# Kernel tuning notes

Hardware: AMD Instinct MI355X
Metric: run time of the kernel (lower is better)

The kernel has to match this reference:

```python
import jax, jax.numpy as jnp
import numpy as np

J = 29  # joints per frame (from fc = Linear(29*3, 2))
C = 3   # feature channels (GCNConv(3, 3))


def setup_inputs() -> dict:
    key = jax.random.key(0)
    ks = jax.random.split(key, 6)
    batch_size, num_frames = 256, 1024
    n_total = batch_size * num_frames * J
    x = jax.random.normal(ks[0], (n_total, C), dtype=jnp.float32)
    edge_index = jax.random.randint(ks[1], (2, 56), 0, J, dtype=jnp.int64)
    # GCNConv(3,3) params and fc Linear(87,2) params
    W = jax.random.normal(ks[2], (C, C), dtype=jnp.float32) / np.sqrt(C)
    b = jnp.zeros((C,), dtype=jnp.float32)
    fc_W = jax.random.normal(ks[3], (J * C, 2), dtype=jnp.float32) / np.sqrt(J * C)
    fc_b = jnp.zeros((2,), dtype=jnp.float32)
    return {"x": x, "edge_index": edge_index, "batch_size": batch_size,
            "num_frames": num_frames, "W": W, "b": b, "fc_W": fc_W, "fc_b": fc_b}


def reference(x, edge_index, batch_size, num_frames, W, b, fc_W, fc_b):
    num_joints = x.shape[0] // (batch_size * num_frames)  # == J
    F = batch_size * num_frames
    self_idx = jnp.arange(num_joints, dtype=edge_index.dtype)
    src = jnp.concatenate([edge_index[0], self_idx])  # add self loops (PyG default)
    dst = jnp.concatenate([edge_index[1], self_idx])
    # symmetric degree normalization D^{-1/2}(A+I)D^{-1/2}
    deg = jnp.zeros((num_joints,), x.dtype).at[dst].add(1.0)
    dinv = jnp.where(deg > 0, jax.lax.rsqrt(deg), 0.0)
    norm = dinv[src] * dinv[dst]  # [E+J]
    # transform then aggregate, vectorized over all frames at once
    xw = (x @ W).reshape(F, num_joints, -1)  # [F, J, C]
    msgs = xw[:, src, :] * norm[None, :, None]  # [F, E+J, C]
    agg = jnp.zeros_like(xw).at[:, dst, :].add(msgs) + b  # scatter-add to targets
    h = jax.nn.relu(agg).reshape(batch_size, num_frames, num_joints * W.shape[1])
    h = jnp.mean(h, axis=1)  # [B, J*C] mean over frames
    z = jax.nn.sigmoid(h @ fc_W + fc_b)  # [B, 2]
    return (h, z)
```

## Files before the change

### kernel.cpp

```cpp
#include <hip/hip_runtime.h>
#include <math.h>

#define J   29
#define CH  3
#define JC  87
#define E0  56
#define B   256
#define T   1024
#define FRAMES (B*T)
#define FPC 64
#define CPB 4
#define NBLK (FRAMES/(FPC*CPB))
#define CHUNK_FLOATS (FPC*JC)
#define CHUNK_BYTES (CHUNK_FLOATS*4)
#define BPB (T/(FPC*CPB))
#define SLOTS 6
#define PROWS 32
#define MAXOV 96
#define WAVES 8
#define RPW 4

typedef const __attribute__((address_space(1))) void* gas_p;
typedef __attribute__((address_space(3))) void* las_p;

__global__ void prep_kernel(const int* __restrict__ ei,
                            int2* __restrict__ pairs,
                            int*  __restrict__ ov_rp,
                            int2* __restrict__ ov_pairs)
{
    __shared__ float M[J * J];
    __shared__ float dinv[J];
    __shared__ int   cnt_ov[J];
    int tid = threadIdx.x;

    for (int i = tid; i < J * J; i += 64) M[i] = 0.f;
    if (tid < J) {
        int d = 1;
        for (int e = 0; e < E0; ++e) d += (ei[E0 + e] == tid) ? 1 : 0;
        dinv[tid] = rsqrtf((float)d);
    }
    __syncthreads();

    if (tid < J) {
        for (int e = 0; e < E0; ++e) {
            if (ei[E0 + e] == tid) {
                int s = ei[e];
                M[tid * J + s] += dinv[s] * dinv[tid];
            }
        }
        M[tid * J + tid] += dinv[tid] * dinv[tid];
        int c = 0;
        for (int i = 0; i < J; ++i) c += (M[tid * J + i] != 0.f) ? 1 : 0;
        cnt_ov[tid] = (c > SLOTS) ? (c - SLOTS) : 0;
    }
    __syncthreads();

    if (tid == 0) {
        int a = 0;
        for (int j = 0; j < J; ++j) { ov_rp[j] = a; a += cnt_ov[j]; }
        for (int j = J; j <= 32; ++j) ov_rp[j] = a;
    }
    __syncthreads();

    if (tid < PROWS) {
        int2 zero; zero.x = 0; zero.y = 0;
        if (tid < J) {
            int s = 0, p = ov_rp[tid];
            for (int i = 0; i < J; ++i) {
                float v = M[tid * J + i];
                if (v != 0.f) {
                    if (s < SLOTS) {
                        int2 pr; pr.x = i * 12; pr.y = __float_as_int(v);
                        pairs[tid * SLOTS + s] = pr;
                    } else {
                        int2 pr; pr.x = (tid << 16) | (i * 12); pr.y = __float_as_int(v);
                        ov_pairs[p++] = pr;
                    }
                    ++s;
                }
            }
            for (; s < SLOTS; ++s) pairs[tid * SLOTS + s] = zero;
        } else {
            for (int s = 0; s < SLOTS; ++s) pairs[tid * SLOTS + s] = zero;
        }
    }
}

__launch_bounds__(512, 6)
__global__ void gcn_main(const float* __restrict__ x,
                         const float* __restrict__ Wp,
                         const float* __restrict__ bp,
                         const int2* __restrict__ pairs,
                         const int*  __restrict__ ov_rp,
                         const int2* __restrict__ ov_pairs,
                         float* __restrict__ partials) {
    __shared__ float xs[CHUNK_FLOATS];

    int tid  = threadIdx.x;
    int lane = tid & 63;
    int wv   = tid >> 6;
    int rowbase = __builtin_amdgcn_readfirstlane(wv * RPW);

    float sW[9], sb[CH];
#pragma unroll
    for (int i = 0; i < 9; ++i) sW[i] = Wp[i];
#pragma unroll
    for (int i = 0; i < CH; ++i) sb[i] = bp[i];
    int ov0 = ov_rp[rowbase], ov1 = ov_rp[rowbase + RPW];

    const char* src = (const char*)(x + (size_t)blockIdx.x * (CPB * CHUNK_FLOATS));
    char* dst = (char*)xs;

    float acc[RPW][CH];
#pragma unroll
    for (int r = 0; r < RPW; ++r)
#pragma unroll
        for (int c = 0; c < CH; ++c) acc[r][c] = 0.f;

    for (int c = 0; c < CPB; ++c) {
        __syncthreads();
        const char* s = src + (size_t)c * CHUNK_BYTES;
        for (int r = wv; r < 22; r += WAVES) {
            int off = (r < 21) ? r * 1024 : 21248;
            __builtin_amdgcn_global_load_lds((gas_p)(s + off + lane * 16),
                                             (las_p)(dst + off), 16, 0, 0);
        }
        asm volatile("s_waitcnt vmcnt(0)" ::: "memory");
        __syncthreads();

        const char* xf = (const char*)xs + lane * (JC * 4);

        float y[RPW][CH];
#pragma unroll
        for (int R = 0; R < RPW; ++R) {
            float a0 = 0.f, a1 = 0.f, a2 = 0.f;
#pragma unroll
            for (int sl = 0; sl < SLOTS; ++sl) {
                int2 pr = pairs[(rowbase + R) * SLOTS + sl];
                float v = __int_as_float(pr.y);
                const float* q = (const float*)(xf + pr.x);
                a0 += v * q[0];
                a1 += v * q[1];
                a2 += v * q[2];
            }
            y[R][0] = a0; y[R][1] = a1; y[R][2] = a2;
        }

        for (int e = ov0; e < ov1; ++e) {
            int2 pr = ov_pairs[e];
            int row = pr.x >> 16;
            int off = pr.x & 0xFFFF;
            float v = __int_as_float(pr.y);
            const float* q = (const float*)(xf + off);
            float d0 = v * q[0], d1 = v * q[1], d2 = v * q[2];
#pragma unroll
            for (int R = 0; R < RPW; ++R) {
                if (row == rowbase + R) {
                    y[R][0] += d0; y[R][1] += d1; y[R][2] += d2;
                }
            }
        }

#pragma unroll
        for (int R = 0; R < RPW; ++R)
#pragma unroll
            for (int ch = 0; ch < CH; ++ch) {
                float t = y[R][0] * sW[0 * CH + ch]
                        + y[R][1] * sW[1 * CH + ch]
                        + y[R][2] * sW[2 * CH + ch]
                        + sb[ch];
                acc[R][ch] += fmaxf(t, 0.f);
            }
    }

#pragma unroll
    for (int R = 0; R < RPW; ++R)
#pragma unroll
        for (int ch = 0; ch < CH; ++ch) {
            float v = acc[R][ch];
#pragma unroll
            for (int m = 1; m < 64; m <<= 1) v += __shfl_xor(v, m, 64);
            acc[R][ch] = v;
        }
    if (lane == 0) {
#pragma unroll
        for (int R = 0; R < RPW; ++R) {
            int j = rowbase + R;
            if (j < J) {
#pragma unroll
                for (int ch = 0; ch < CH; ++ch)
                    partials[(size_t)blockIdx.x * JC + j * CH + ch] = acc[R][ch];
            }
        }
    }
}

__global__ void finalize_kernel(const float* __restrict__ partials,
                                const float* __restrict__ fcW,
                                const float* __restrict__ fcb,
                                float* __restrict__ out) {
    __shared__ float h[JC];
    int b = blockIdx.x, tid = threadIdx.x;
    if (tid < JC) {
        float a = 0.f;
#pragma unroll
        for (int p = 0; p < BPB; ++p)
            a += partials[(size_t)(b * BPB + p) * JC + tid];
        a *= (1.0f / (float)T);
        h[tid] = a;
        out[(size_t)b * JC + tid] = a;
    }
    __syncthreads();
    if (tid < 2) {
        float a = fcb[tid];
        for (int r = 0; r < JC; ++r) a += h[r] * fcW[r * 2 + tid];
        out[(size_t)B * JC + b * 2 + tid] = 1.0f / (1.0f + expf(-a));
    }
}

extern "C" void kernel_launch(void* const* d_in, const int* in_sizes, int n_in,
                              void* d_out, int out_size, void* d_ws, size_t ws_size,
                              hipStream_t stream) {
    const float* x   = (const float*)d_in[0];
    const int*   ei  = (const int*)d_in[1];
    const float* W   = (const float*)d_in[4];
    const float* bb  = (const float*)d_in[5];
    const float* fcW = (const float*)d_in[6];
    const float* fcb = (const float*)d_in[7];

    char* ws = (char*)d_ws;
    int2* pairs    = (int2*)ws;
    int2* ov_pairs = pairs + PROWS * SLOTS;
    int*  ov_rp    = (int*)(ov_pairs + MAXOV);
    float* partials = (float*)(ws + 4096);

    prep_kernel<<<1, 64, 0, stream>>>(ei, pairs, ov_rp, ov_pairs);
    gcn_main<<<NBLK, WAVES * 64, 0, stream>>>(x, W, bb, pairs, ov_rp, ov_pairs, partials);
    finalize_kernel<<<B, 128, 0, stream>>>(partials, fcW, fcb, (float*)d_out);
}
```

Baseline: 44.35 us.

## Pad joints to float4 in LDS via strided async loads, shrink slot count

The async global-to-LDS copy now loads each joint's 12-byte triple into its own 16-byte slot. This lets the aggregation read one aligned float4 per neighbour instead of three scalar LDS reads at a 12-byte stride. It uses more copy rounds and more LDS per block. The last chunk of the last block gets special handling so the load does not read past the end of the buffer. SLOTS also drops from 6 to 4, so more neighbours go through the overflow loop, and unused overflow entries are now zero-filled.

```diff
diff --git a/kernel.cpp b/kernel.cpp
--- a/kernel.cpp
+++ b/kernel.cpp
@@ -14,11 +14,12 @@
 #define CHUNK_FLOATS (FPC*JC)
 #define CHUNK_BYTES (CHUNK_FLOATS*4)
 #define BPB (T/(FPC*CPB))
-#define SLOTS 6
+#define SLOTS 4
 #define PROWS 32
 #define MAXOV 96
 #define WAVES 8
 #define RPW 4
+#define NROUND 29
 
 typedef const __attribute__((address_space(1))) void* gas_p;
 typedef __attribute__((address_space(3))) void* las_p;
@@ -70,10 +71,10 @@
                 float v = M[tid * J + i];
                 if (v != 0.f) {
                     if (s < SLOTS) {
-                        int2 pr; pr.x = i * 12; pr.y = __float_as_int(v);
+                        int2 pr; pr.x = i * 16; pr.y = __float_as_int(v);
                         pairs[tid * SLOTS + s] = pr;
                     } else {
-                        int2 pr; pr.x = (tid << 16) | (i * 12); pr.y = __float_as_int(v);
+                        int2 pr; pr.x = (tid << 16) | (i * 16); pr.y = __float_as_int(v);
                         ov_pairs[p++] = pr;
                     }
                     ++s;
@@ -83,6 +84,11 @@
         } else {
             for (int s = 0; s < SLOTS; ++s) pairs[tid * SLOTS + s] = zero;
         }
+    }
+    __syncthreads();
+    if (tid == 0) {
+        int a = ov_rp[J];
+        for (int i = a; i < MAXOV; ++i) { int2 pr; pr.x = 0; pr.y = 0; ov_pairs[i] = pr; }
     }
 }
 
@@ -94,7 +100,7 @@
                          const int*  __restrict__ ov_rp,
                          const int2* __restrict__ ov_pairs,
                          float* __restrict__ partials) {
-    __shared__ float xs[CHUNK_FLOATS];
+    __shared__ float4 xs4[FPC * J];
 
     int tid  = threadIdx.x;
     int lane = tid & 63;
@@ -109,7 +115,8 @@
     int ov0 = ov_rp[rowbase], ov1 = ov_rp[rowbase + RPW];
 
     const char* src = (const char*)(x + (size_t)blockIdx.x * (CPB * CHUNK_FLOATS));
-    char* dst = (char*)xs;
+    char* dst = (char*)xs4;
+    const bool lastBlock = (blockIdx.x == NBLK - 1);
 
     float acc[RPW][CH];
 #pragma unroll
@@ -120,15 +127,23 @@
     for (int c = 0; c < CPB; ++c) {
         __syncthreads();
         const char* s = src + (size_t)c * CHUNK_BYTES;
-        for (int r = wv; r < 22; r += WAVES) {
-            int off = (r < 21) ? r * 1024 : 21248;
-            __builtin_amdgcn_global_load_lds((gas_p)(s + off + lane * 16),
-                                             (las_p)(dst + off), 16, 0, 0);
+        const bool lastChunk = lastBlock && (c == CPB - 1);
+        for (int r = wv; r < NROUND; r += WAVES) {
+            int goff = r * 768 + lane * 12;
+            if (lastChunk && r == NROUND - 1)
+                goff = (goff > CHUNK_BYTES - 16) ? (CHUNK_BYTES - 16) : goff;
+            __builtin_amdgcn_global_load_lds((gas_p)(s + goff),
+                                             (las_p)(dst + r * 1024), 16, 0, 0);
         }
         asm volatile("s_waitcnt vmcnt(0)" ::: "memory");
+        if (lastChunk && wv == (NROUND - 1) % WAVES && lane == 0) {
+            volatile float* slot = (volatile float*)(xs4 + (FPC * J - 1));
+            float a = slot[1], b2 = slot[2], c2 = slot[3];
+            slot[0] = a; slot[1] = b2; slot[2] = c2;
+        }
         __syncthreads();
 
-        const char* xf = (const char*)xs + lane * (JC * 4);
+        const char* xf = (const char*)xs4 + lane * (J * 16);
 
         float y[RPW][CH];
 #pragma unroll
@@ -138,10 +153,10 @@
             for (int sl = 0; sl < SLOTS; ++sl) {
                 int2 pr = pairs[(rowbase + R) * SLOTS + sl];
                 float v = __int_as_float(pr.y);
-                const float* q = (const float*)(xf + pr.x);
-                a0 += v * q[0];
-                a1 += v * q[1];
-                a2 += v * q[2];
+                float4 q = *(const float4*)(xf + pr.x);
+                a0 += v * q.x;
+                a1 += v * q.y;
+                a2 += v * q.z;
             }
             y[R][0] = a0; y[R][1] = a1; y[R][2] = a2;
         }
@@ -151,8 +166,8 @@
             int row = pr.x >> 16;
             int off = pr.x & 0xFFFF;
             float v = __int_as_float(pr.y);
-            const float* q = (const float*)(xf + off);
-            float d0 = v * q[0], d1 = v * q[1], d2 = v * q[2];
+            float4 q = *(const float4*)(xf + off);
+            float d0 = v * q.x, d1 = v * q.y, d2 = v * q.z;
 #pragma unroll
             for (int R = 0; R < RPW; ++R) {
                 if (row == rowbase + R) {
```

Result: no change. 44.07 us (-0.6%).

## Fuse prep, main and finalize into one per-batch kernel with multi-buffered LDS prefetch

Applied to the files above, without the earlier changes.

Replaces the three-kernel pipeline with a single kernel where each block processes one batch element's 1024 frames. Input chunks are streamed into a 5-slot LDS ring with asynchronous global-to-LDS loads issued several chunks ahead, using partial vmcnt waits. Adjacency weights are computed per wave in registers/LDS instead of a separate prep kernel, and the frame mean plus fc/sigmoid is done in-block, removing the partials round trip and extra launches. It trades occupancy (large LDS, fewer blocks) for deeper memory-level parallelism and fewer launches.

```diff
diff --git a/kernel.cpp b/kernel.cpp
--- a/kernel.cpp
+++ b/kernel.cpp
@@ -1,115 +1,117 @@
 #include <hip/hip_runtime.h>
 #include <math.h>
 
-#define J   29
-#define CH  3
-#define JC  87
-#define E0  56
-#define B   256
-#define T   1024
-#define FRAMES (B*T)
-#define FPC 64
-#define CPB 4
-#define NBLK (FRAMES/(FPC*CPB))
-#define CHUNK_FLOATS (FPC*JC)
-#define CHUNK_BYTES (CHUNK_FLOATS*4)
-#define BPB (T/(FPC*CPB))
-#define SLOTS 6
-#define PROWS 32
-#define MAXOV 96
+#define J     29
+#define CH    3
+#define JC    87
+#define E0    56
+#define BATCH 256
+#define T     1024
+#define FPC   64
+#define CPB   16
+#define CHUNK_BYTES (FPC*JC*4)
+#define LDSCH 22528
+#define NBUF  5
+#define DEPTH 4
 #define WAVES 8
-#define RPW 4
+#define RPW   4
+#define NROUND 22
+#define OVCAP 64
 
 typedef const __attribute__((address_space(1))) void* gas_p;
 typedef __attribute__((address_space(3))) void* las_p;
 
-__global__ void prep_kernel(const int* __restrict__ ei,
-                            int2* __restrict__ pairs,
-                            int*  __restrict__ ov_rp,
-                            int2* __restrict__ ov_pairs)
-{
-    __shared__ float M[J * J];
-    __shared__ float dinv[J];
-    __shared__ int   cnt_ov[J];
-    int tid = threadIdx.x;
-
-    for (int i = tid; i < J * J; i += 64) M[i] = 0.f;
-    if (tid < J) {
-        int d = 1;
-        for (int e = 0; e < E0; ++e) d += (ei[E0 + e] == tid) ? 1 : 0;
-        dinv[tid] = rsqrtf((float)d);
-    }
-    __syncthreads();
-
-    if (tid < J) {
-        for (int e = 0; e < E0; ++e) {
-            if (ei[E0 + e] == tid) {
-                int s = ei[e];
-                M[tid * J + s] += dinv[s] * dinv[tid];
-            }
-        }
-        M[tid * J + tid] += dinv[tid] * dinv[tid];
-        int c = 0;
-        for (int i = 0; i < J; ++i) c += (M[tid * J + i] != 0.f) ? 1 : 0;
-        cnt_ov[tid] = (c > SLOTS) ? (c - SLOTS) : 0;
-    }
-    __syncthreads();
-
-    if (tid == 0) {
-        int a = 0;
-        for (int j = 0; j < J; ++j) { ov_rp[j] = a; a += cnt_ov[j]; }
-        for (int j = J; j <= 32; ++j) ov_rp[j] = a;
-    }
-    __syncthreads();
-
-    if (tid < PROWS) {
-        int2 zero; zero.x = 0; zero.y = 0;
-        if (tid < J) {
-            int s = 0, p = ov_rp[tid];
-            for (int i = 0; i < J; ++i) {
-                float v = M[tid * J + i];
-                if (v != 0.f) {
-                    if (s < SLOTS) {
-                        int2 pr; pr.x = i * 12; pr.y = __float_as_int(v);
-                        pairs[tid * SLOTS + s] = pr;
-                    } else {
-                        int2 pr; pr.x = (tid << 16) | (i * 12); pr.y = __float_as_int(v);
-                        ov_pairs[p++] = pr;
-                    }
-                    ++s;
-                }
-            }
-            for (; s < SLOTS; ++s) pairs[tid * SLOTS + s] = zero;
-        } else {
-            for (int s = 0; s < SLOTS; ++s) pairs[tid * SLOTS + s] = zero;
+__device__ __forceinline__ void stage_chunk(const char* __restrict__ s,
+                                            char* d, int lane, int wv,
+                                            bool lastChunk) {
+#pragma unroll
+    for (int r0 = 0; r0 < 3; ++r0) {
+        int r = wv + WAVES * r0;
+        if (r < NROUND) {
+            int goff = r * 1024 + lane * 16;
+            if (lastChunk && goff > CHUNK_BYTES - 16) goff = CHUNK_BYTES - 16;
+            __builtin_amdgcn_global_load_lds((gas_p)(s + goff),
+                                             (las_p)(d + r * 1024), 16, 0, 0);
         }
     }
 }
 
-__launch_bounds__(512, 6)
-__global__ void gcn_main(const float* __restrict__ x,
-                         const float* __restrict__ Wp,
-                         const float* __restrict__ bp,
-                         const int2* __restrict__ pairs,
-                         const int*  __restrict__ ov_rp,
-                         const int2* __restrict__ ov_pairs,
-                         float* __restrict__ partials) {
-    __shared__ float xs[CHUNK_FLOATS];
+__global__ __launch_bounds__(512)
+void gcn_fused(const float* __restrict__ x,
+               const int*   __restrict__ ei,
+               const float* __restrict__ Wp,
+               const float* __restrict__ bp,
+               const float* __restrict__ fcW,
+               const float* __restrict__ fcb,
+               float* __restrict__ out) {
+    __shared__ __align__(16) char ldsx[NBUF * LDSCH];
+    __shared__ int2  s_ov[WAVES * OVCAP];
+    __shared__ float h_s[32 * CH];
 
     int tid  = threadIdx.x;
     int lane = tid & 63;
     int wv   = tid >> 6;
-    int rowbase = __builtin_amdgcn_readfirstlane(wv * RPW);
-
-    float sW[9], sb[CH];
-#pragma unroll
-    for (int i = 0; i < 9; ++i) sW[i] = Wp[i];
-#pragma unroll
-    for (int i = 0; i < CH; ++i) sb[i] = bp[i];
-    int ov0 = ov_rp[rowbase], ov1 = ov_rp[rowbase + RPW];
-
-    const char* src = (const char*)(x + (size_t)blockIdx.x * (CPB * CHUNK_FLOATS));
-    char* dst = (char*)xs;
+    int rowbase = wv * RPW;
+
+    const char* src = (const char*)x + (size_t)blockIdx.x * ((size_t)CPB * CHUNK_BYTES);
+    const bool lastBlock = (blockIdx.x == BATCH - 1);
+
+#pragma unroll
+    for (int c = 0; c < DEPTH; ++c)
+        stage_chunk(src + (size_t)c * CHUNK_BYTES, ldsx + c * LDSCH, lane, wv, false);
+
+    float dinv = 0.f;
+    if (lane < J) {
+        int d = 1;
+        for (int e = 0; e < E0; ++e) d += (ei[E0 + e] == lane) ? 1 : 0;
+        dinv = rsqrtf((float)d);
+    }
+    float mrow[RPW];
+    int   prx[RPW][4];
+    float prv[RPW][4];
+    int ovn = 0;
+#pragma unroll
+    for (int R = 0; R < RPW; ++R) {
+        int j = rowbase + R;
+        float mv = 0.f;
+        if (lane < J && j < J) {
+            int cnt = 0;
+            for (int e = 0; e < E0; ++e)
+                cnt += (ei[e] == lane && ei[E0 + e] == j) ? 1 : 0;
+            float dj = __shfl(dinv, j);
+            mv = (float)cnt * dinv * dj;
+            if (lane == j) mv += dinv * dinv;
+        }
+        mrow[R] = mv;
+        unsigned long long mask = __ballot(mv != 0.f);
+#pragma unroll
+        for (int sl = 0; sl < 4; ++sl) {
+            int pos = 0; float v = 0.f;
+            if (mask) {
+                pos = __ffsll(mask) - 1;
+                v = __shfl(mrow[R], pos);
+                mask &= mask - 1;
+            }
+            prx[R][sl] = pos * 12;
+            prv[R][sl] = v;
+        }
+        while (mask) {
+            int pos = __ffsll(mask) - 1;
+            mask &= mask - 1;
+            float v = __shfl(mrow[R], pos);
+            if (lane == 0) {
+                int2 pr; pr.x = (j << 16) | (pos * 12); pr.y = __float_as_int(v);
+                s_ov[wv * OVCAP + ovn] = pr;
+            }
+            ++ovn;
+        }
+    }
+    float sWv[9], sbv[CH];
+#pragma unroll
+    for (int i = 0; i < 9; ++i) sWv[i] = Wp[i];
+#pragma unroll
+    for (int i = 0; i < CH; ++i) sbv[i] = bp[i];
+    asm volatile("s_waitcnt lgkmcnt(0)" ::: "memory");
 
     float acc[RPW][CH];
 #pragma unroll
@@ -118,57 +120,59 @@
         for (int c = 0; c < CH; ++c) acc[r][c] = 0.f;
 
     for (int c = 0; c < CPB; ++c) {
-        __syncthreads();
-        const char* s = src + (size_t)c * CHUNK_BYTES;
-        for (int r = wv; r < 22; r += WAVES) {
-            int off = (r < 21) ? r * 1024 : 21248;
-            __builtin_amdgcn_global_load_lds((gas_p)(s + off + lane * 16),
-                                             (las_p)(dst + off), 16, 0, 0);
-        }
-        asm volatile("s_waitcnt vmcnt(0)" ::: "memory");
-        __syncthreads();
-
-        const char* xf = (const char*)xs + lane * (JC * 4);
+        asm volatile("" ::: "memory");
+        __builtin_amdgcn_s_barrier();
+        asm volatile("" ::: "memory");
+
+        if (c + DEPTH < CPB) {
+            stage_chunk(src + (size_t)(c + DEPTH) * CHUNK_BYTES,
+                        ldsx + ((c + DEPTH) % NBUF) * LDSCH, lane, wv,
+                        lastBlock && (c + DEPTH == CPB - 1));
+            if (wv < 6) asm volatile("s_waitcnt vmcnt(12)" ::: "memory");
+            else        asm volatile("s_waitcnt vmcnt(8)"  ::: "memory");
+        } else {
+            asm volatile("s_waitcnt vmcnt(0)" ::: "memory");
+        }
+
+        asm volatile("" ::: "memory");
+        __builtin_amdgcn_s_barrier();
+        __builtin_amdgcn_sched_barrier(0);
+
+        const char* xf = ldsx + (c % NBUF) * LDSCH + lane * (JC * 4);
 
         float y[RPW][CH];
 #pragma unroll
         for (int R = 0; R < RPW; ++R) {
             float a0 = 0.f, a1 = 0.f, a2 = 0.f;
 #pragma unroll
-            for (int sl = 0; sl < SLOTS; ++sl) {
-                int2 pr = pairs[(rowbase + R) * SLOTS + sl];
-                float v = __int_as_float(pr.y);
-                const float* q = (const float*)(xf + pr.x);
+            for (int sl = 0; sl < 4; ++sl) {
+                float v = prv[R][sl];
+                const float* q = (const float*)(xf + prx[R][sl]);
                 a0 += v * q[0];
                 a1 += v * q[1];
                 a2 += v * q[2];
             }
             y[R][0] = a0; y[R][1] = a1; y[R][2] = a2;
         }
-
-        for (int e = ov0; e < ov1; ++e) {
-            int2 pr = ov_pairs[e];
+        for (int e = 0; e < ovn; ++e) {
+            int2 pr = s_ov[wv * OVCAP + e];
             int row = pr.x >> 16;
             int off = pr.x & 0xFFFF;
             float v = __int_as_float(pr.y);
             const float* q = (const float*)(xf + off);
             float d0 = v * q[0], d1 = v * q[1], d2 = v * q[2];
 #pragma unroll
-            for (int R = 0; R < RPW; ++R) {
-                if (row == rowbase + R) {
-                    y[R][0] += d0; y[R][1] += d1; y[R][2] += d2;
-                }
-            }
-        }
-
+            for (int R = 0; R < RPW; ++R)
+                if (row == rowbase + R) { y[R][0] += d0; y[R][1] += d1; y[R][2] += d2; }
+        }
 #pragma unroll
         for (int R = 0; R < RPW; ++R)
 #pragma unroll
             for (int ch = 0; ch < CH; ++ch) {
-                float t = y[R][0] * sW[0 * CH + ch]
-                        + y[R][1] * sW[1 * CH + ch]
-                        + y[R][2] * sW[2 * CH + ch]
-                        + sb[ch];
+                float t = y[R][0] * sWv[0 * CH + ch]
+                        + y[R][1] * sWv[1 * CH + ch]
+                        + y[R][2] * sWv[2 * CH + ch]
+                        + sbv[ch];
                 acc[R][ch] += fmaxf(t, 0.f);
             }
     }
@@ -179,42 +183,18 @@
         for (int ch = 0; ch < CH; ++ch) {
             float v = acc[R][ch];
 #pragma unroll
-            for (int m = 1; m < 64; m <<= 1) v += __shfl_xor(v, m, 64);
-            acc[R][ch] = v;
-        }
-    if (lane == 0) {
-#pragma unroll
-        for (int R = 0; R < RPW; ++R) {
-            int j = rowbase + R;
-            if (j < J) {
-#pragma unroll
-                for (int ch = 0; ch < CH; ++ch)
-                    partials[(size_t)blockIdx.x * JC + j * CH + ch] = acc[R][ch];
-            }
-        }
-    }
-}
-
-__global__ void finalize_kernel(const float* __restrict__ partials,
-                                const float* __restrict__ fcW,
-                                const float* __restrict__ fcb,
-                                float* __restrict__ out) {
-    __shared__ float h[JC];
-    int b = blockIdx.x, tid = threadIdx.x;
-    if (tid < JC) {
-        float a = 0.f;
-#pragma unroll
-        for (int p = 0; p < BPB; ++p)
-            a += partials[(size_t)(b * BPB + p) * JC + tid];
-        a *= (1.0f / (float)T);
-        h[tid] = a;
-        out[(size_t)b * JC + tid] = a;
-    }
+            for (int s = 1; s < 64; s <<= 1) v += __shfl_xor(v, s, 64);
+            if (lane == 0 && (rowbase + R) < J) h_s[(rowbase + R) * CH + ch] = v;
+        }
     __syncthreads();
+
+    int b = blockIdx.x;
+    if (tid < JC) out[(size_t)b * JC + tid] = h_s[tid] * (1.0f / (float)T);
     if (tid < 2) {
         float a = fcb[tid];
-        for (int r = 0; r < JC; ++r) a += h[r] * fcW[r * 2 + tid];
-        out[(size_t)B * JC + b * 2 + tid] = 1.0f / (1.0f + expf(-a));
+        for (int r = 0; r < JC; ++r)
+            a += h_s[r] * (1.0f / (float)T) * fcW[r * 2 + tid];
+        out[(size_t)BATCH * JC + b * 2 + tid] = 1.0f / (1.0f + expf(-a));
     }
 }
 
@@ -228,13 +208,5 @@
     const float* fcW = (const float*)d_in[6];
     const float* fcb = (const float*)d_in[7];
 
-    char* ws = (char*)d_ws;
-    int2* pairs    = (int2*)ws;
-    int2* ov_pairs = pairs + PROWS * SLOTS;
-    int*  ov_rp    = (int*)(ov_pairs + MAXOV);
-    float* partials = (float*)(ws + 4096);
-
-    prep_kernel<<<1, 64, 0, stream>>>(ei, pairs, ov_rp, ov_pairs);
-    gcn_main<<<NBLK, WAVES * 64, 0, stream>>>(x, W, bb, pairs, ov_rp, ov_pairs, partials);
-    finalize_kernel<<<B, 128, 0, stream>>>(partials, fcW, fcb, (float*)d_out);
+    gcn_fused<<<BATCH, WAVES * 64, 0, stream>>>(x, ei, W, bb, fcW, fcb, (float*)d_out);
 }
```

Measured after the change: 46.65 us. +5.2%, slower.

## Register-prefetch next chunk, cache pairs in registers and overflow list in LDS

Applied to the files above, without the earlier changes.

Replaces the direct global-to-LDS async loads with a register prefetch pipeline: the next chunk is loaded into float4 registers while the current chunk is computed, then stored to LDS. The per-row pair table is held in registers, SLOTS drops from 6 to 4 so more edges go to an overflow list kept in LDS, and the final wave shuffle reduction becomes an LDS column sum. Occupancy hint raised to 8 blocks. The aim is to overlap memory latency with compute and remove repeated global loads of pair data, at the cost of extra register pressure and more overflow-loop iterations.

```diff
diff --git a/kernel.cpp b/kernel.cpp
--- a/kernel.cpp
+++ b/kernel.cpp
@@ -11,17 +11,14 @@
 #define FPC 64
 #define CPB 4
 #define NBLK (FRAMES/(FPC*CPB))
-#define CHUNK_FLOATS (FPC*JC)
-#define CHUNK_BYTES (CHUNK_FLOATS*4)
+#define CHUNK_F4 1392
 #define BPB (T/(FPC*CPB))
-#define SLOTS 6
+#define SLOTS 4
 #define PROWS 32
 #define MAXOV 96
 #define WAVES 8
 #define RPW 4
-
-typedef const __attribute__((address_space(1))) void* gas_p;
-typedef __attribute__((address_space(3))) void* las_p;
+#define PFN 3
 
 __global__ void prep_kernel(const int* __restrict__ ei,
                             int2* __restrict__ pairs,
@@ -84,17 +81,23 @@
             for (int s = 0; s < SLOTS; ++s) pairs[tid * SLOTS + s] = zero;
         }
     }
-}
-
-__launch_bounds__(512, 6)
-__global__ void gcn_main(const float* __restrict__ x,
-                         const float* __restrict__ Wp,
-                         const float* __restrict__ bp,
-                         const int2* __restrict__ pairs,
-                         const int*  __restrict__ ov_rp,
-                         const int2* __restrict__ ov_pairs,
-                         float* __restrict__ partials) {
-    __shared__ float xs[CHUNK_FLOATS];
+    __syncthreads();
+    if (tid == 0) {
+        int a = ov_rp[J];
+        for (int i = a; i < MAXOV; ++i) { int2 pr; pr.x = 0; pr.y = 0; ov_pairs[i] = pr; }
+    }
+}
+
+__global__ __launch_bounds__(512, 8)
+void gcn_main(const float* __restrict__ x,
+              const float* __restrict__ Wp,
+              const float* __restrict__ bp,
+              const int2* __restrict__ pairs,
+              const int*  __restrict__ ov_rp,
+              const int2* __restrict__ ov_pairs,
+              float* __restrict__ partials) {
+    __shared__ float4 xs4[CHUNK_F4];
+    __shared__ int2   s_ov[MAXOV];
 
     int tid  = threadIdx.x;
     int lane = tid & 63;
@@ -107,9 +110,22 @@
 #pragma unroll
     for (int i = 0; i < CH; ++i) sb[i] = bp[i];
     int ov0 = ov_rp[rowbase], ov1 = ov_rp[rowbase + RPW];
-
-    const char* src = (const char*)(x + (size_t)blockIdx.x * (CPB * CHUNK_FLOATS));
-    char* dst = (char*)xs;
+    int2 pr_[RPW][SLOTS];
+#pragma unroll
+    for (int R = 0; R < RPW; ++R)
+#pragma unroll
+        for (int sl = 0; sl < SLOTS; ++sl)
+            pr_[R][sl] = pairs[(rowbase + R) * SLOTS + sl];
+    if (tid < MAXOV) s_ov[tid] = ov_pairs[tid];
+
+    const float4* src4 = (const float4*)x + (size_t)blockIdx.x * (CPB * CHUNK_F4);
+
+    float4 pf[PFN];
+#pragma unroll
+    for (int k = 0; k < PFN; ++k) {
+        int idx = k * 512 + tid; if (idx > CHUNK_F4 - 1) idx = CHUNK_F4 - 1;
+        pf[k] = src4[idx];
+    }
 
     float acc[RPW][CH];
 #pragma unroll
@@ -117,18 +133,26 @@
 #pragma unroll
         for (int c = 0; c < CH; ++c) acc[r][c] = 0.f;
 
+#pragma unroll
     for (int c = 0; c < CPB; ++c) {
         __syncthreads();
-        const char* s = src + (size_t)c * CHUNK_BYTES;
-        for (int r = wv; r < 22; r += WAVES) {
-            int off = (r < 21) ? r * 1024 : 21248;
-            __builtin_amdgcn_global_load_lds((gas_p)(s + off + lane * 16),
-                                             (las_p)(dst + off), 16, 0, 0);
-        }
-        asm volatile("s_waitcnt vmcnt(0)" ::: "memory");
+#pragma unroll
+        for (int k = 0; k < PFN; ++k) {
+            int idx = k * 512 + tid; if (idx > CHUNK_F4 - 1) idx = CHUNK_F4 - 1;
+            xs4[idx] = pf[k];
+        }
         __syncthreads();
 
-        const char* xf = (const char*)xs + lane * (JC * 4);
+        if (c + 1 < CPB) {
+            const float4* s2 = src4 + (c + 1) * CHUNK_F4;
+#pragma unroll
+            for (int k = 0; k < PFN; ++k) {
+                int idx = k * 512 + tid; if (idx > CHUNK_F4 - 1) idx = CHUNK_F4 - 1;
+                pf[k] = s2[idx];
+            }
+        }
+
+        const char* xf = (const char*)xs4 + lane * 348;
 
         float y[RPW][CH];
 #pragma unroll
@@ -136,7 +160,7 @@
             float a0 = 0.f, a1 = 0.f, a2 = 0.f;
 #pragma unroll
             for (int sl = 0; sl < SLOTS; ++sl) {
-                int2 pr = pairs[(rowbase + R) * SLOTS + sl];
+                int2 pr = pr_[R][sl];
                 float v = __int_as_float(pr.y);
                 const float* q = (const float*)(xf + pr.x);
                 a0 += v * q[0];
@@ -145,22 +169,17 @@
             }
             y[R][0] = a0; y[R][1] = a1; y[R][2] = a2;
         }
-
         for (int e = ov0; e < ov1; ++e) {
-            int2 pr = ov_pairs[e];
+            int2 pr = s_ov[e];
             int row = pr.x >> 16;
             int off = pr.x & 0xFFFF;
             float v = __int_as_float(pr.y);
             const float* q = (const float*)(xf + off);
             float d0 = v * q[0], d1 = v * q[1], d2 = v * q[2];
 #pragma unroll
-            for (int R = 0; R < RPW; ++R) {
-                if (row == rowbase + R) {
-                    y[R][0] += d0; y[R][1] += d1; y[R][2] += d2;
-                }
-            }
-        }
-
+            for (int R = 0; R < RPW; ++R)
+                if (row == rowbase + R) { y[R][0] += d0; y[R][1] += d1; y[R][2] += d2; }
+        }
 #pragma unroll
         for (int R = 0; R < RPW; ++R)
 #pragma unroll
@@ -173,25 +192,23 @@
             }
     }
 
-#pragma unroll
-    for (int R = 0; R < RPW; ++R)
-#pragma unroll
-        for (int ch = 0; ch < CH; ++ch) {
-            float v = acc[R][ch];
-#pragma unroll
-            for (int m = 1; m < 64; m <<= 1) v += __shfl_xor(v, m, 64);
-            acc[R][ch] = v;
-        }
-    if (lane == 0) {
-#pragma unroll
-        for (int R = 0; R < RPW; ++R) {
-            int j = rowbase + R;
-            if (j < J) {
-#pragma unroll
-                for (int ch = 0; ch < CH; ++ch)
-                    partials[(size_t)blockIdx.x * JC + j * CH + ch] = acc[R][ch];
-            }
-        }
+    __syncthreads();
+    float* red = (float*)xs4;
+#pragma unroll
+    for (int R = 0; R < RPW; ++R) {
+        int j = rowbase + R;
+        if (j < J) {
+#pragma unroll
+            for (int ch = 0; ch < CH; ++ch)
+                red[lane * JC + j * CH + ch] = acc[R][ch];
+        }
+    }
+    __syncthreads();
+    if (tid < JC) {
+        float a = 0.f;
+#pragma unroll
+        for (int L = 0; L < FPC; ++L) a += red[L * JC + tid];
+        partials[(size_t)blockIdx.x * JC + tid] = a;
     }
 }
 
```

Result: slower. 77.19 us (+74.0%).
